# Optimization experiments

Hardware: AMD Instinct MI355X
Metric: run time of the kernel (lower is better)

## Reference

```python
import jax, jax.numpy as jnp
import numpy as np

B, S, DIM = 2, 2048, 2048
N_HEADS, N_KV_HEADS = 16, 4
HEAD_DIM = DIM // N_HEADS  # 128
N_REP = N_HEADS // N_KV_HEADS  # 4


def setup_inputs() -> dict:
    key = jax.random.key(0)
    ks = jax.random.split(key, 7)
    x = jax.random.normal(ks[0], (B, S, DIM), dtype=jnp.float32)
    cos = jax.random.uniform(ks[1], (S, HEAD_DIM // 2), dtype=jnp.float32)
    sin = jax.random.uniform(ks[2], (S, HEAD_DIM // 2), dtype=jnp.float32)
    sc = 1.0 / np.sqrt(DIM)
    wq = jax.random.normal(ks[3], (DIM, N_HEADS * HEAD_DIM), dtype=jnp.float32) * sc
    wk = jax.random.normal(ks[4], (DIM, N_KV_HEADS * HEAD_DIM), dtype=jnp.float32) * sc
    wv = jax.random.normal(ks[5], (DIM, N_KV_HEADS * HEAD_DIM), dtype=jnp.float32) * sc
    wo = jax.random.normal(ks[6], (N_HEADS * HEAD_DIM, DIM), dtype=jnp.float32) * sc
    return {"x": x, "cos": cos, "sin": sin, "wq": wq, "wk": wk, "wv": wv, "wo": wo}


def _rope(t, cos, sin):
    # t: [B, S, H, hd]; cos/sin: [S, hd/2] -> broadcast as [1, S, 1, hd/2]
    tr, ti = t[..., ::2], t[..., 1::2]
    c = cos[None, :, None, :]
    s = sin[None, :, None, :]
    out_r = tr * c - ti * s
    out_i = tr * s + ti * c
    # interleave back: stack on new last axis then flatten
    return jnp.stack([out_r, out_i], axis=-1).reshape(t.shape)


def reference(x, cos, sin, wq, wk, wv, wo):
    bsz, seqlen, _ = x.shape
    xq = (x @ wq).reshape(bsz, seqlen, N_HEADS, HEAD_DIM)
    xk = (x @ wk).reshape(bsz, seqlen, N_KV_HEADS, HEAD_DIM)
    xv = (x @ wv).reshape(bsz, seqlen, N_KV_HEADS, HEAD_DIM)
    xq = _rope(xq, cos, sin)
    xk = _rope(xk, cos, sin)
    # GQA: repeat kv heads -> [B, S, H, hd]
    xk = jnp.repeat(xk, N_REP, axis=2)
    xv = jnp.repeat(xv, N_REP, axis=2)
    scale = 1.0 / jnp.sqrt(jnp.asarray(HEAD_DIM, dtype=x.dtype))
    scores = jnp.einsum("bqhd,bkhd->bhqk", xq, xk) * scale
    causal = jnp.tril(jnp.ones((seqlen, seqlen), dtype=bool))
    scores = jnp.where(causal[None, None, :, :], scores, jnp.asarray(-jnp.inf, dtype=scores.dtype))
    attn = jax.nn.softmax(scores, axis=-1)
    out = jnp.einsum("bhqk,bkhd->bqhd", attn, xv)
    out = out.reshape(bsz, seqlen, N_HEADS * HEAD_DIM)
    return out @ wo
```

## Files before the change

kernel.cpp:

```cpp
#include <hip/hip_runtime.h>
#include <stdint.h>

#define SEQ 2048

typedef uint16_t u16;
typedef uint32_t u32;
typedef __attribute__((ext_vector_type(4))) float f32x4;
typedef __attribute__((ext_vector_type(8))) __bf16 bf16x8;
typedef __attribute__((ext_vector_type(4))) __bf16 bf16x4;

__device__ __forceinline__ u16 f2bf(float f) {
    u32 u = __float_as_uint(f);
    u += 0x7FFFu + ((u >> 16) & 1u);
    return (u16)(u >> 16);
}
__device__ __forceinline__ float bf2f(u16 h) {
    return __uint_as_float(((u32)h) << 16);
}
__device__ __forceinline__ u32 cvt_pk_bf16(float lo, float hi) {
    u32 r;
    asm("v_cvt_pk_bf16_f32 %0, %1, %2" : "=v"(r) : "v"(lo), "v"(hi));
    return r;
}
__device__ __forceinline__ void async16(const void* g, void* l) {
    auto gp = (__attribute__((address_space(1))) void*)const_cast<void*>(g);
    auto lp = (__attribute__((address_space(3))) void*)l;
    __builtin_amdgcn_global_load_lds(gp, lp, 16, 0, 0);
}

__global__ __launch_bounds__(256) void convert_bf16(const float* __restrict__ src,
                                                    u16* __restrict__ dst) {
    int i = blockIdx.x * 256 + threadIdx.x;
    float4 v = ((const float4*)src)[i];
    ((uint2*)dst)[i] = make_uint2(cvt_pk_bf16(v.x, v.y), cvt_pk_bf16(v.z, v.w));
}

__global__ __launch_bounds__(256) void tconv_all(const float* __restrict__ wq,
                                                 const float* __restrict__ wk,
                                                 const float* __restrict__ wv,
                                                 const float* __restrict__ wo,
                                                 u16* __restrict__ wqkvT,
                                                 u16* __restrict__ woT) {
    __shared__ float tile[64][65];
    const int bx = blockIdx.x, k0 = blockIdx.y * 64;
    const float* src; u16* dst; int N, n0;
    if (bx < 32)      { src = wq; dst = wqkvT;                        N = 2048; n0 = bx * 64; }
    else if (bx < 40) { src = wk; dst = wqkvT + (size_t)2048 * 2048;  N = 512;  n0 = (bx - 32) * 64; }
    else if (bx < 48) { src = wv; dst = wqkvT + (size_t)2560 * 2048;  N = 512;  n0 = (bx - 40) * 64; }
    else              { src = wo; dst = woT;                          N = 2048; n0 = (bx - 48) * 64; }
    const int tid = threadIdx.x;
#pragma unroll
    for (int p = 0; p < 4; p++) {
        int r = p * 16 + (tid >> 4);
        int c = (tid & 15) * 4;
        float4 v = *(const float4*)&src[(size_t)(k0 + r) * N + n0 + c];
        tile[r][c] = v.x; tile[r][c+1] = v.y; tile[r][c+2] = v.z; tile[r][c+3] = v.w;
    }
    __syncthreads();
#pragma unroll
    for (int p = 0; p < 4; p++) {
        int n = p * 16 + (tid >> 4);
        int kq = (tid & 15) * 4;
        u32 lo = cvt_pk_bf16(tile[kq+0][n], tile[kq+1][n]);
        u32 hi = cvt_pk_bf16(tile[kq+2][n], tile[kq+3][n]);
        *(uint2*)&dst[(size_t)(n0 + n) * 2048 + k0 + kq] = make_uint2(lo, hi);
    }
}

template <bool FUSE>
__global__ __launch_bounds__(256, 2) void gemm128(const u16* __restrict__ A,
                                                  const u16* __restrict__ Bt,
                                                  void* __restrict__ Cv,
                                                  int N, int K, int nbx,
                                                  const float* __restrict__ cosp,
                                                  const float* __restrict__ sinp,
                                                  u16* __restrict__ vt) {
    __shared__ u16 lds[4 * 8192];

    const int nwg = gridDim.x;
    const int q = nwg >> 3, r = nwg & 7;
    const int xcd = blockIdx.x & 7, lid = blockIdx.x >> 3;
    const int wg = (xcd < r ? xcd * (q + 1) : r * (q + 1) + (xcd - r) * q) + lid;
    const int by = wg / nbx, bx = wg - by * nbx;
    const int m0 = by * 128, n0 = bx * 128;

    const int tid = threadIdx.x;
    const int w = tid >> 6, l = tid & 63;
    const int lr = l & 15, quad = l >> 4;
    const int wm = (w >> 1) * 64, wn = (w & 1) * 64;
    const int cs = ((quad ^ (lr & 3) ^ ((lr >> 2) & 3)) & 3) * 8;

    const int sr = tid >> 2;
    const int sg = tid & 3;
    const int swz = (sr ^ (sr >> 2)) & 3;
    const u16* aS = A  + (size_t)(m0 + sr) * K + (sg ^ swz) * 8;
    const u16* bS = Bt + (size_t)(n0 + sr) * K + (sg ^ swz) * 8;
    u16* ldA = lds + tid * 8;
    u16* ldB = lds + 4096 + tid * 8;

    f32x4 acc[4][4] = {};
    const int nK = K >> 5;

    auto stage = [&](int kt) {
        u16* dA = ldA + (kt & 3) * 8192;
        u16* dB = ldB + (kt & 3) * 8192;
        const u16* sa = aS + (size_t)kt * 32;
        const u16* sb = bS + (size_t)kt * 32;
        async16(sa, dA);
        async16(sa + (size_t)64 * K, dA + 2048);
        async16(sb, dB);
        async16(sb + (size_t)64 * K, dB + 2048);
    };

    stage(0); stage(1); stage(2);
    asm volatile("s_waitcnt vmcnt(8)" ::: "memory");
    __builtin_amdgcn_s_barrier();

    for (int kt = 0; kt < nK; ++kt) {
        const u16* As = lds + (kt & 3) * 8192;
        const u16* Bs = As + 4096;
        bf16x8 af[4], bfr[4];
#pragma unroll
        for (int i = 0; i < 4; i++)
            af[i] = *(const bf16x8*)&As[(wm + i * 16 + lr) * 32 + cs];
#pragma unroll
        for (int i = 0; i < 4; i++)
            bfr[i] = *(const bf16x8*)&Bs[(wn + i * 16 + lr) * 32 + cs];
        if (kt + 3 < nK) stage(kt + 3);
        __builtin_amdgcn_s_barrier();
        asm volatile("s_waitcnt lgkmcnt(0)" ::: "memory");
        __builtin_amdgcn_s_setprio(1);
#pragma unroll
        for (int mf = 0; mf < 4; mf++)
#pragma unroll
            for (int nf = 0; nf < 4; nf++)
                acc[mf][nf] = __builtin_amdgcn_mfma_f32_16x16x32_bf16(af[mf], bfr[nf], acc[mf][nf], 0, 0, 0);
        __builtin_amdgcn_s_setprio(0);
        if (kt < nK - 3)       asm volatile("s_waitcnt vmcnt(8)" ::: "memory");
        else if (kt == nK - 3) asm volatile("s_waitcnt vmcnt(4)" ::: "memory");
        else if (kt == nK - 2) asm volatile("s_waitcnt vmcnt(0)" ::: "memory");
        if (kt < nK - 1) __builtin_amdgcn_s_barrier();
    }

    if constexpr (FUSE) {
        if (n0 >= 2560) {
            const int bb = m0 >> 11;
#pragma unroll
            for (int mf = 0; mf < 4; mf++) {
                const int token0 = (m0 + wm + mf * 16 + quad * 4) & (SEQ - 1);
#pragma unroll
                for (int nf = 0; nf < 4; nf++) {
                    int dg = n0 - 2560 + wn + nf * 16 + lr;
                    int kh = dg >> 7, d = dg & 127;
                    u32 lo = cvt_pk_bf16(acc[mf][nf][0], acc[mf][nf][1]);
                    u32 hi = cvt_pk_bf16(acc[mf][nf][2], acc[mf][nf][3]);
                    *(uint2*)&vt[((size_t)((bb * 4 + kh) * 128 + d)) * SEQ + token0] = make_uint2(lo, hi);
                }
            }
        } else if (n0 >= 2048) {
            const float sgn = (lr & 1) ? 1.0f : -1.0f;
#pragma unroll
            for (int mf = 0; mf < 4; mf++) {
#pragma unroll
                for (int nf = 0; nf < 4; nf++) {
                    int col = n0 + wn + nf * 16 + lr;
                    int ci = (col & 127) >> 1;
#pragma unroll
                    for (int rr = 0; rr < 4; rr++) {
                        size_t row = (size_t)(m0 + wm + mf * 16 + quad * 4 + rr);
                        int token = (int)row & (SEQ - 1);
                        float v = acc[mf][nf][rr];
                        float ppart = __shfl_xor(v, 1);
                        float c = cosp[token * 64 + ci];
                        float s = sinp[token * 64 + ci];
                        float ov = fmaf(sgn * ppart, s, v * c);
                        ((u16*)Cv)[row * (size_t)N + col] = f2bf(ov);
                    }
                }
            }
        } else {
#pragma unroll
            for (int mf = 0; mf < 4; mf++)
#pragma unroll
                for (int nf = 0; nf < 4; nf++)
#pragma unroll
                    for (int rr = 0; rr < 4; rr++) {
                        size_t row = (size_t)(m0 + wm + mf * 16 + quad * 4 + rr);
                        size_t col = (size_t)(n0 + wn + nf * 16 + lr);
                        ((u16*)Cv)[row * (size_t)N + col] = f2bf(acc[mf][nf][rr]);
                    }
        }
    } else {
#pragma unroll
        for (int mf = 0; mf < 4; mf++)
#pragma unroll
            for (int nf = 0; nf < 4; nf++)
#pragma unroll
                for (int rr = 0; rr < 4; rr++) {
                    size_t row = (size_t)(m0 + wm + mf * 16 + quad * 4 + rr);
                    size_t col = (size_t)(n0 + wn + nf * 16 + lr);
                    ((float*)Cv)[row * (size_t)N + col] = acc[mf][nf][rr];
                }
    }
}

__global__ __launch_bounds__(512, 2) void flash_attn(const u16* __restrict__ qkv,
                                                     const u16* __restrict__ vt,
                                                     const float* __restrict__ cosp,
                                                     const float* __restrict__ sinp,
                                                     u16* __restrict__ ob) {
    __shared__ u16 sh[65536];
    const int bidx = blockIdx.x;
    const int xcd   = bidx & 7;
    const int inner = bidx >> 3;
    const int b  = xcd >> 2, kh = xcd & 3;
    const int h  = kh * 4 + (inner & 3);
    const int a  = inner >> 2;
    const int tid = threadIdx.x;
    const int w = tid >> 6, lane = tid & 63;
    const int grp = w >> 2, wl = w & 3;
    const int lr = lane & 15, quad = lane >> 4;
    const float qscale = 0.088388347762f * 1.4426950408889634f;

    u16* base_g = sh + grp * 24576;
    u16* vb  = base_g + 16384;
    u16* lPw = sh + 49152 + w * 2048;

    const int tidg = tid & 255;
    const int krow = tidg >> 4;
    const int kchunk = (tidg & 15) ^ krow;
    const int vrow = tidg >> 3;
    const int vchunk = (tidg & 7) ^ (vrow & 7);
    const u16* kRow = qkv + (size_t)b * SEQ * 3072 + 2048 + kh * 128
                    + (size_t)krow * 3072 + kchunk * 8;
    const u16* vRow = vt + (size_t)(b * 4 + kh) * 128 * SEQ
                    + (size_t)vrow * SEQ + vchunk * 8;

    auto stageK = [&](int kt, int buf) {
        u16* d = base_g + buf * 8192 + tidg * 8;
#pragma unroll
        for (int i = 0; i < 4; i++)
            async16(kRow + (size_t)(kt * 64 + i * 16) * 3072, d + i * 2048);
    };
    auto stageV = [&](int kt) {
        u16* d = vb + tidg * 8;
#pragma unroll
        for (int i = 0; i < 4; i++)
            async16(vRow + (size_t)(i * 32) * SEQ + kt * 64, d + i * 2048);
    };

    float* mO = (float*)sh;
    float* mM = (float*)(sh + 49152);

    for (int p = 0; p < 2; p++) {
        const int qt = p ? (7 - a) : (8 + a);
        const int niters = p ? (8 - a) : (9 + a);
        const int kt0 = grp * niters;

        stageK(kt0, 0);

        bf16x8 qf[2][4];
#pragma unroll
        for (int qi = 0; qi < 2; qi++) {
            const int token = qt * 128 + wl * 32 + qi * 16 + lr;
            const u16* qb = qkv + (size_t)(b * SEQ + token) * 3072 + h * 128;
#pragma unroll
            for (int kk = 0; kk < 4; kk++) {
                uint4 raw = *(const uint4*)(qb + kk * 32 + quad * 8);
                u32 rw[4] = {raw.x, raw.y, raw.z, raw.w};
                union { u32 u[4]; bf16x8 v; } fr;
#pragma unroll
                for (int pp = 0; pp < 4; pp++) {
                    int ci = kk * 16 + quad * 4 + pp;
                    float cv = cosp[token * 64 + ci];
                    float sv = sinp[token * 64 + ci];
                    float tr = bf2f((u16)(rw[pp] & 0xFFFFu));
                    float ti = bf2f((u16)(rw[pp] >> 16));
                    fr.u[pp] = cvt_pk_bf16((tr * cv - ti * sv) * qscale,
                                           (tr * sv + ti * cv) * qscale);
                }
                qf[qi][kk] = fr.v;
            }
        }

        f32x4 o[2][8] = {};
        float m_st[2] = {-1e30f, -1e30f};
        float l_st[2] = {0.f, 0.f};
        const int qg = qt * 128 + wl * 32 + lr;

        for (int t = 0; t < niters; t++) {
            const int kt = kt0 + t;
            const int buf = t & 1;
            stageV(kt);
            if (t + 1 < niters) {
                stageK(kt + 1, buf ^ 1);
                asm volatile("s_waitcnt vmcnt(8)" ::: "memory");
            } else {
                asm volatile("s_waitcnt vmcnt(4)" ::: "memory");
            }
            asm volatile("s_barrier" ::: "memory");

            const u16* kcur = base_g + buf * 8192;
            f32x4 sc[2][4] = {};
            __builtin_amdgcn_s_setprio(1);
#pragma unroll
            for (int nf = 0; nf < 4; nf++) {
#pragma unroll
                for (int kk = 0; kk < 4; kk++) {
                    bf16x8 ak = *(const bf16x8*)&kcur[(nf * 16 + lr) * 128 + (((kk * 4 + quad) ^ lr) * 8)];
                    sc[0][nf] = __builtin_amdgcn_mfma_f32_16x16x32_bf16(ak, qf[0][kk], sc[0][nf], 0, 0, 0);
                    sc[1][nf] = __builtin_amdgcn_mfma_f32_16x16x32_bf16(ak, qf[1][kk], sc[1][nf], 0, 0, 0);
                }
            }
            __builtin_amdgcn_s_setprio(0);

            const int kb = kt * 64 + quad * 4;
            const int kmax = kt * 64 + 63;
#pragma unroll
            for (int qi = 0; qi < 2; qi++) {
                float ps[4][4];
                float tm[4];
                const int qrow_g = qg + qi * 16;
                if (kmax > qt * 128 + wl * 32 + qi * 16) {
#pragma unroll
                    for (int nf = 0; nf < 4; nf++) {
                        tm[nf] = -1e30f;
#pragma unroll
                        for (int r = 0; r < 4; r++) {
                            float v = sc[qi][nf][r];
                            if ((kb + nf * 16 + r) > qrow_g) v = -1e30f;
                            ps[nf][r] = v;
                            tm[nf] = fmaxf(tm[nf], v);
                        }
                    }
                } else {
#pragma unroll
                    for (int nf = 0; nf < 4; nf++) {
                        tm[nf] = -1e30f;
#pragma unroll
                        for (int r = 0; r < 4; r++) {
                            float v = sc[qi][nf][r];
                            ps[nf][r] = v;
                            tm[nf] = fmaxf(tm[nf], v);
                        }
                    }
                }
                float tmax = fmaxf(fmaxf(tm[0], tm[1]), fmaxf(tm[2], tm[3]));
                tmax = fmaxf(tmax, __shfl_xor(tmax, 16));
                tmax = fmaxf(tmax, __shfl_xor(tmax, 32));
                const float mprev = m_st[qi];
                if (!__all(tmax - mprev <= 8.0f)) {
                    float mnew = fmaxf(mprev, tmax);
                    float alpha = exp2f(mprev - mnew);
                    l_st[qi] *= alpha;
                    m_st[qi] = mnew;
#pragma unroll
                    for (int r = 0; r < 4; r++) {
                        float ar = __shfl(alpha, quad * 4 + r, 16);
#pragma unroll
                        for (int nd = 0; nd < 8; nd++) o[qi][nd][r] *= ar;
                    }
                }
                const float mcur = m_st[qi];
                float rs[4];
#pragma unroll
                for (int nf = 0; nf < 4; nf++) {
                    rs[nf] = 0.f;
#pragma unroll
                    for (int r = 0; r < 4; r++) {
                        float e = exp2f(ps[nf][r] - mcur);
                        ps[nf][r] = e;
                        rs[nf] += e;
                    }
                }
                float rsum = (rs[0] + rs[1]) + (rs[2] + rs[3]);
                rsum += __shfl_xor(rsum, 16);
                rsum += __shfl_xor(rsum, 32);
                l_st[qi] += rsum;
                const int qrow = qi * 16 + lr;
#pragma unroll
                for (int nf = 0; nf < 4; nf++) {
                    u32 lo = cvt_pk_bf16(ps[nf][0], ps[nf][1]);
                    u32 hi = cvt_pk_bf16(ps[nf][2], ps[nf][3]);
                    int c = (nf * 4 + quad) ^ lr;
                    *(uint2*)&lPw[qrow * 64 + c * 4] = make_uint2(lo, hi);
                }
            }

            if (t + 1 < niters) asm volatile("s_waitcnt vmcnt(4)" ::: "memory");
            else                asm volatile("s_waitcnt vmcnt(0)" ::: "memory");
            asm volatile("s_barrier" ::: "memory");

            __builtin_amdgcn_s_setprio(1);
#pragma unroll
            for (int kf = 0; kf < 2; kf++) {
                bf16x8 pa[2];
#pragma unroll
                for (int qi = 0; qi < 2; qi++) {
                    int c0 = (kf * 8 + quad * 2) ^ lr;
                    int c1 = (kf * 8 + quad * 2 + 1) ^ lr;
                    bf16x4 p0 = *(const bf16x4*)&lPw[(qi * 16 + lr) * 64 + c0 * 4];
                    bf16x4 p1 = *(const bf16x4*)&lPw[(qi * 16 + lr) * 64 + c1 * 4];
                    pa[qi] = __builtin_shufflevector(p0, p1, 0, 1, 2, 3, 4, 5, 6, 7);
                }
#pragma unroll
                for (int nd = 0; nd < 8; nd++) {
                    bf16x8 vv = *(const bf16x8*)&vb[(nd * 16 + lr) * 64 + (((kf * 4 + quad) ^ (lr & 7)) * 8)];
                    o[0][nd] = __builtin_amdgcn_mfma_f32_16x16x32_bf16(pa[0], vv, o[0][nd], 0, 0, 0);
                    o[1][nd] = __builtin_amdgcn_mfma_f32_16x16x32_bf16(pa[1], vv, o[1][nd], 0, 0, 0);
                }
            }
            __builtin_amdgcn_s_setprio(0);

            asm volatile("s_barrier" ::: "memory");
        }

        __syncthreads();
        if (grp == 1) {
#pragma unroll
            for (int qi = 0; qi < 2; qi++) {
#pragma unroll
                for (int r = 0; r < 4; r++) {
                    int row = wl * 32 + qi * 16 + quad * 4 + r;
#pragma unroll
                    for (int nd = 0; nd < 8; nd++)
                        mO[row * 128 + nd * 16 + lr] = o[qi][nd][r];
                }
                if (quad == 0) {
                    int rowl = wl * 32 + qi * 16 + lr;
                    mM[rowl * 2]     = m_st[qi];
                    mM[rowl * 2 + 1] = l_st[qi];
                }
            }
        }
        __syncthreads();
        if (grp == 0) {
#pragma unroll
            for (int qi = 0; qi < 2; qi++) {
                int rowl = wl * 32 + qi * 16 + lr;
                float m1 = mM[rowl * 2], l1 = mM[rowl * 2 + 1];
                float M  = fmaxf(m_st[qi], m1);
                float a0 = exp2f(m_st[qi] - M);
                float a1 = exp2f(m1 - M);
                float li = 1.0f / (l_st[qi] * a0 + l1 * a1);
                u16* obase = ob + (size_t)(b * SEQ + qt * 128 + wl * 32 + qi * 16) * 2048 + h * 128;
#pragma unroll
                for (int r = 0; r < 4; r++) {
                    float a0b = __shfl(a0, quad * 4 + r, 16);
                    float a1b = __shfl(a1, quad * 4 + r, 16);
                    float lib = __shfl(li, quad * 4 + r, 16);
                    int row = wl * 32 + qi * 16 + quad * 4 + r;
#pragma unroll
                    for (int nd = 0; nd < 8; nd++) {
                        float val = (o[qi][nd][r] * a0b + mO[row * 128 + nd * 16 + lr] * a1b) * lib;
                        obase[(quad * 4 + r) * 2048 + nd * 16 + lr] = f2bf(val);
                    }
                }
            }
        }
        __syncthreads();
    }
}

extern "C" void kernel_launch(void* const* d_in, const int* in_sizes, int n_in,
                              void* d_out, int out_size, void* d_ws, size_t ws_size,
                              hipStream_t stream) {
    (void)in_sizes; (void)n_in; (void)out_size; (void)ws_size;
    const float* x    = (const float*)d_in[0];
    const float* cosp = (const float*)d_in[1];
    const float* sinp = (const float*)d_in[2];
    const float* wq   = (const float*)d_in[3];
    const float* wk   = (const float*)d_in[4];
    const float* wv   = (const float*)d_in[5];
    const float* wo   = (const float*)d_in[6];
    float* out = (float*)d_out;

    char* ws = (char*)d_ws;
    u16* xb    = (u16*)(ws);
    u16* qkvb  = (u16*)(ws + (size_t)16 * 1024 * 1024);
    u16* wqkvT = (u16*)(ws + (size_t)40 * 1024 * 1024);
    u16* woT   = (u16*)(ws + (size_t)52 * 1024 * 1024);
    u16* vtb   = (u16*)(ws + (size_t)60 * 1024 * 1024);
    u16* ob    = xb;

    convert_bf16<<<8192, 256, 0, stream>>>(x, xb);
    tconv_all<<<dim3(80, 32), 256, 0, stream>>>(wq, wk, wv, wo, wqkvT, woT);
    gemm128<true><<<768, 256, 0, stream>>>(xb, wqkvT, (void*)qkvb, 3072, 2048, 24,
                                           cosp, sinp, vtb);
    flash_attn<<<256, 512, 0, stream>>>(qkvb, vtb, cosp, sinp, ob);
    gemm128<false><<<512, 256, 0, stream>>>(ob, woT, (void*)out, 2048, 2048, 16,
                                            nullptr, nullptr, nullptr);
}
```

Baseline: 308.4 us.

## Replace split-KV two-group attention blocks with one q-tile per 256-thread block

The attention kernel previously used 512-thread blocks in which two wave groups split the KV range of a query tile, handled two paired q-tiles per block for load balance, and merged partial results through shared memory. Now each 256-thread block handles one 128-row q-tile over the full causal KV range, with 512 blocks ordered so heavy and light tiles interleave. This removes the cross-group merge, the extra syncthreads and half the shared memory. In exchange, per-block work becomes unbalanced (from 2 to 32 iterations), so tail effects depend on how the scheduler packs blocks.

Result: no change. 311.7 us (+1.1%).

```diff
diff --git a/kernel.cpp b/kernel.cpp
--- a/kernel.cpp
+++ b/kernel.cpp
@@ -204,261 +204,220 @@
     }
 }
 
-__global__ __launch_bounds__(512, 2) void flash_attn(const u16* __restrict__ qkv,
+__global__ __launch_bounds__(256, 2) void flash_attn(const u16* __restrict__ qkv,
                                                      const u16* __restrict__ vt,
                                                      const float* __restrict__ cosp,
                                                      const float* __restrict__ sinp,
                                                      u16* __restrict__ ob) {
-    __shared__ u16 sh[65536];
+    __shared__ u16 sh[32768];
     const int bidx = blockIdx.x;
     const int xcd   = bidx & 7;
     const int inner = bidx >> 3;
     const int b  = xcd >> 2, kh = xcd & 3;
-    const int h  = kh * 4 + (inner & 3);
-    const int a  = inner >> 2;
+    const int c  = inner & 31;
+    const int qt = (inner >> 5) ? (15 - (c >> 2)) : (c >> 2);
+    const int h  = kh * 4 + (c & 3);
     const int tid = threadIdx.x;
     const int w = tid >> 6, lane = tid & 63;
-    const int grp = w >> 2, wl = w & 3;
     const int lr = lane & 15, quad = lane >> 4;
     const float qscale = 0.088388347762f * 1.4426950408889634f;
 
-    u16* base_g = sh + grp * 24576;
-    u16* vb  = base_g + 16384;
-    u16* lPw = sh + 49152 + w * 2048;
-
-    const int tidg = tid & 255;
-    const int krow = tidg >> 4;
-    const int kchunk = (tidg & 15) ^ krow;
-    const int vrow = tidg >> 3;
-    const int vchunk = (tidg & 7) ^ (vrow & 7);
+    u16* vb  = sh + 16384;
+    u16* lPw = sh + 24576 + w * 2048;
+
+    const int krow = tid >> 4;
+    const int kchunk = (tid & 15) ^ krow;
+    const int vrow = tid >> 3;
+    const int vchunk = (tid & 7) ^ (vrow & 7);
     const u16* kRow = qkv + (size_t)b * SEQ * 3072 + 2048 + kh * 128
                     + (size_t)krow * 3072 + kchunk * 8;
     const u16* vRow = vt + (size_t)(b * 4 + kh) * 128 * SEQ
                     + (size_t)vrow * SEQ + vchunk * 8;
 
     auto stageK = [&](int kt, int buf) {
-        u16* d = base_g + buf * 8192 + tidg * 8;
+        u16* d = sh + buf * 8192 + tid * 8;
 #pragma unroll
         for (int i = 0; i < 4; i++)
             async16(kRow + (size_t)(kt * 64 + i * 16) * 3072, d + i * 2048);
     };
     auto stageV = [&](int kt) {
-        u16* d = vb + tidg * 8;
+        u16* d = vb + tid * 8;
 #pragma unroll
         for (int i = 0; i < 4; i++)
             async16(vRow + (size_t)(i * 32) * SEQ + kt * 64, d + i * 2048);
     };
 
-    float* mO = (float*)sh;
-    float* mM = (float*)(sh + 49152);
-
-    for (int p = 0; p < 2; p++) {
-        const int qt = p ? (7 - a) : (8 + a);
-        const int niters = p ? (8 - a) : (9 + a);
-        const int kt0 = grp * niters;
-
-        stageK(kt0, 0);
-
-        bf16x8 qf[2][4];
+    const int niters = 2 * (qt + 1);
+
+    stageK(0, 0);
+
+    bf16x8 qf[2][4];
+#pragma unroll
+    for (int qi = 0; qi < 2; qi++) {
+        const int token = qt * 128 + w * 32 + qi * 16 + lr;
+        const u16* qb = qkv + (size_t)(b * SEQ + token) * 3072 + h * 128;
+#pragma unroll
+        for (int kk = 0; kk < 4; kk++) {
+            uint4 raw = *(const uint4*)(qb + kk * 32 + quad * 8);
+            u32 rw[4] = {raw.x, raw.y, raw.z, raw.w};
+            union { u32 u[4]; bf16x8 v; } fr;
+#pragma unroll
+            for (int pp = 0; pp < 4; pp++) {
+                int ci = kk * 16 + quad * 4 + pp;
+                float cv = cosp[token * 64 + ci];
+                float sv = sinp[token * 64 + ci];
+                float tr = bf2f((u16)(rw[pp] & 0xFFFFu));
+                float ti = bf2f((u16)(rw[pp] >> 16));
+                fr.u[pp] = cvt_pk_bf16((tr * cv - ti * sv) * qscale,
+                                       (tr * sv + ti * cv) * qscale);
+            }
+            qf[qi][kk] = fr.v;
+        }
+    }
+
+    f32x4 o[2][8] = {};
+    float m_st[2] = {-1e30f, -1e30f};
+    float l_st[2] = {0.f, 0.f};
+    const int qg = qt * 128 + w * 32 + lr;
+
+    for (int t = 0; t < niters; t++) {
+        const int kt = t;
+        const int buf = t & 1;
+        stageV(kt);
+        if (t + 1 < niters) {
+            stageK(kt + 1, buf ^ 1);
+            asm volatile("s_waitcnt vmcnt(8)" ::: "memory");
+        } else {
+            asm volatile("s_waitcnt vmcnt(4)" ::: "memory");
+        }
+        asm volatile("s_barrier" ::: "memory");
+
+        const u16* kcur = sh + buf * 8192;
+        f32x4 sc[2][4] = {};
+        __builtin_amdgcn_s_setprio(1);
+#pragma unroll
+        for (int nf = 0; nf < 4; nf++) {
+#pragma unroll
+            for (int kk = 0; kk < 4; kk++) {
+                bf16x8 ak = *(const bf16x8*)&kcur[(nf * 16 + lr) * 128 + (((kk * 4 + quad) ^ lr) * 8)];
+                sc[0][nf] = __builtin_amdgcn_mfma_f32_16x16x32_bf16(ak, qf[0][kk], sc[0][nf], 0, 0, 0);
+                sc[1][nf] = __builtin_amdgcn_mfma_f32_16x16x32_bf16(ak, qf[1][kk], sc[1][nf], 0, 0, 0);
+            }
+        }
+        __builtin_amdgcn_s_setprio(0);
+
+        const int kb = kt * 64 + quad * 4;
+        const int kmax = kt * 64 + 63;
 #pragma unroll
         for (int qi = 0; qi < 2; qi++) {
-            const int token = qt * 128 + wl * 32 + qi * 16 + lr;
-            const u16* qb = qkv + (size_t)(b * SEQ + token) * 3072 + h * 128;
-#pragma unroll
-            for (int kk = 0; kk < 4; kk++) {
-                uint4 raw = *(const uint4*)(qb + kk * 32 + quad * 8);
-                u32 rw[4] = {raw.x, raw.y, raw.z, raw.w};
-                union { u32 u[4]; bf16x8 v; } fr;
-#pragma unroll
-                for (int pp = 0; pp < 4; pp++) {
-                    int ci = kk * 16 + quad * 4 + pp;
-                    float cv = cosp[token * 64 + ci];
-                    float sv = sinp[token * 64 + ci];
-                    float tr = bf2f((u16)(rw[pp] & 0xFFFFu));
-                    float ti = bf2f((u16)(rw[pp] >> 16));
-                    fr.u[pp] = cvt_pk_bf16((tr * cv - ti * sv) * qscale,
-                                           (tr * sv + ti * cv) * qscale);
-                }
-                qf[qi][kk] = fr.v;
-            }
-        }
-
-        f32x4 o[2][8] = {};
-        float m_st[2] = {-1e30f, -1e30f};
-        float l_st[2] = {0.f, 0.f};
-        const int qg = qt * 128 + wl * 32 + lr;
-
-        for (int t = 0; t < niters; t++) {
-            const int kt = kt0 + t;
-            const int buf = t & 1;
-            stageV(kt);
-            if (t + 1 < niters) {
-                stageK(kt + 1, buf ^ 1);
-                asm volatile("s_waitcnt vmcnt(8)" ::: "memory");
+            float ps[4][4];
+            float tm[4];
+            const int qrow_g = qg + qi * 16;
+            if (kmax > qt * 128 + w * 32 + qi * 16) {
+#pragma unroll
+                for (int nf = 0; nf < 4; nf++) {
+                    tm[nf] = -1e30f;
+#pragma unroll
+                    for (int r = 0; r < 4; r++) {
+                        float v = sc[qi][nf][r];
+                        if ((kb + nf * 16 + r) > qrow_g) v = -1e30f;
+                        ps[nf][r] = v;
+                        tm[nf] = fmaxf(tm[nf], v);
+                    }
+                }
             } else {
-                asm volatile("s_waitcnt vmcnt(4)" ::: "memory");
-            }
-            asm volatile("s_barrier" ::: "memory");
-
-            const u16* kcur = base_g + buf * 8192;
-            f32x4 sc[2][4] = {};
-            __builtin_amdgcn_s_setprio(1);
+#pragma unroll
+                for (int nf = 0; nf < 4; nf++) {
+                    tm[nf] = -1e30f;
+#pragma unroll
+                    for (int r = 0; r < 4; r++) {
+                        float v = sc[qi][nf][r];
+                        ps[nf][r] = v;
+                        tm[nf] = fmaxf(tm[nf], v);
+                    }
+                }
+            }
+            float tmax = fmaxf(fmaxf(tm[0], tm[1]), fmaxf(tm[2], tm[3]));
+            tmax = fmaxf(tmax, __shfl_xor(tmax, 16));
+            tmax = fmaxf(tmax, __shfl_xor(tmax, 32));
+            const float mprev = m_st[qi];
+            if (!__all(tmax - mprev <= 8.0f)) {
+                float mnew = fmaxf(mprev, tmax);
+                float alpha = exp2f(mprev - mnew);
+                l_st[qi] *= alpha;
+                m_st[qi] = mnew;
+#pragma unroll
+                for (int r = 0; r < 4; r++) {
+                    float ar = __shfl(alpha, quad * 4 + r, 16);
+#pragma unroll
+                    for (int nd = 0; nd < 8; nd++) o[qi][nd][r] *= ar;
+                }
+            }
+            const float mcur = m_st[qi];
+            float rs[4];
 #pragma unroll
             for (int nf = 0; nf < 4; nf++) {
-#pragma unroll
-                for (int kk = 0; kk < 4; kk++) {
-                    bf16x8 ak = *(const bf16x8*)&kcur[(nf * 16 + lr) * 128 + (((kk * 4 + quad) ^ lr) * 8)];
-                    sc[0][nf] = __builtin_amdgcn_mfma_f32_16x16x32_bf16(ak, qf[0][kk], sc[0][nf], 0, 0, 0);
-                    sc[1][nf] = __builtin_amdgcn_mfma_f32_16x16x32_bf16(ak, qf[1][kk], sc[1][nf], 0, 0, 0);
-                }
-            }
-            __builtin_amdgcn_s_setprio(0);
-
-            const int kb = kt * 64 + quad * 4;
-            const int kmax = kt * 64 + 63;
+                rs[nf] = 0.f;
+#pragma unroll
+                for (int r = 0; r < 4; r++) {
+                    float e = exp2f(ps[nf][r] - mcur);
+                    ps[nf][r] = e;
+                    rs[nf] += e;
+                }
+            }
+            float rsum = (rs[0] + rs[1]) + (rs[2] + rs[3]);
+            rsum += __shfl_xor(rsum, 16);
+            rsum += __shfl_xor(rsum, 32);
+            l_st[qi] += rsum;
+            const int qrow = qi * 16 + lr;
+#pragma unroll
+            for (int nf = 0; nf < 4; nf++) {
+                u32 lo = cvt_pk_bf16(ps[nf][0], ps[nf][1]);
+                u32 hi = cvt_pk_bf16(ps[nf][2], ps[nf][3]);
+                int cc = (nf * 4 + quad) ^ lr;
+                *(uint2*)&lPw[qrow * 64 + cc * 4] = make_uint2(lo, hi);
+            }
+        }
+
+        if (t + 1 < niters) asm volatile("s_waitcnt vmcnt(4)" ::: "memory");
+        else                asm volatile("s_waitcnt vmcnt(0)" ::: "memory");
+        asm volatile("s_barrier" ::: "memory");
+
+        __builtin_amdgcn_s_setprio(1);
+#pragma unroll
+        for (int kf = 0; kf < 2; kf++) {
+            bf16x8 pa[2];
 #pragma unroll
             for (int qi = 0; qi < 2; qi++) {
-                float ps[4][4];
-                float tm[4];
-                const int qrow_g = qg + qi * 16;
-                if (kmax > qt * 128 + wl * 32 + qi * 16) {
-#pragma unroll
-                    for (int nf = 0; nf < 4; nf++) {
-                        tm[nf] = -1e30f;
-#pragma unroll
-                        for (int r = 0; r < 4; r++) {
-                            float v = sc[qi][nf][r];
-                            if ((kb + nf * 16 + r) > qrow_g) v = -1e30f;
-                            ps[nf][r] = v;
-                            tm[nf] = fmaxf(tm[nf], v);
-                        }
-                    }
-                } else {
-#pragma unroll
-                    for (int nf = 0; nf < 4; nf++) {
-                        tm[nf] = -1e30f;
-#pragma unroll
-                        for (int r = 0; r < 4; r++) {
-                            float v = sc[qi][nf][r];
-                            ps[nf][r] = v;
-                            tm[nf] = fmaxf(tm[nf], v);
-                        }
-                    }
-                }
-                float tmax = fmaxf(fmaxf(tm[0], tm[1]), fmaxf(tm[2], tm[3]));
-                tmax = fmaxf(tmax, __shfl_xor(tmax, 16));
-                tmax = fmaxf(tmax, __shfl_xor(tmax, 32));
-                const float mprev = m_st[qi];
-                if (!__all(tmax - mprev <= 8.0f)) {
-                    float mnew = fmaxf(mprev, tmax);
-                    float alpha = exp2f(mprev - mnew);
-                    l_st[qi] *= alpha;
-                    m_st[qi] = mnew;
-#pragma unroll
-                    for (int r = 0; r < 4; r++) {
-                        float ar = __shfl(alpha, quad * 4 + r, 16);
-#pragma unroll
-                        for (int nd = 0; nd < 8; nd++) o[qi][nd][r] *= ar;
-                    }
-                }
-                const float mcur = m_st[qi];
-                float rs[4];
-#pragma unroll
-                for (int nf = 0; nf < 4; nf++) {
-                    rs[nf] = 0.f;
-#pragma unroll
-                    for (int r = 0; r < 4; r++) {
-                        float e = exp2f(ps[nf][r] - mcur);
-                        ps[nf][r] = e;
-                        rs[nf] += e;
-                    }
-                }
-                float rsum = (rs[0] + rs[1]) + (rs[2] + rs[3]);
-                rsum += __shfl_xor(rsum, 16);
-                rsum += __shfl_xor(rsum, 32);
-                l_st[qi] += rsum;
-                const int qrow = qi * 16 + lr;
-#pragma unroll
-                for (int nf = 0; nf < 4; nf++) {
-                    u32 lo = cvt_pk_bf16(ps[nf][0], ps[nf][1]);
-                    u32 hi = cvt_pk_bf16(ps[nf][2], ps[nf][3]);
-                    int c = (nf * 4 + quad) ^ lr;
-                    *(uint2*)&lPw[qrow * 64 + c * 4] = make_uint2(lo, hi);
-                }
-            }
-
-            if (t + 1 < niters) asm volatile("s_waitcnt vmcnt(4)" ::: "memory");
-            else                asm volatile("s_waitcnt vmcnt(0)" ::: "memory");
-            asm volatile("s_barrier" ::: "memory");
-
-            __builtin_amdgcn_s_setprio(1);
-#pragma unroll
-            for (int kf = 0; kf < 2; kf++) {
-                bf16x8 pa[2];
-#pragma unroll
-                for (int qi = 0; qi < 2; qi++) {
-                    int c0 = (kf * 8 + quad * 2) ^ lr;
-                    int c1 = (kf * 8 + quad * 2 + 1) ^ lr;
-                    bf16x4 p0 = *(const bf16x4*)&lPw[(qi * 16 + lr) * 64 + c0 * 4];
-                    bf16x4 p1 = *(const bf16x4*)&lPw[(qi * 16 + lr) * 64 + c1 * 4];
-                    pa[qi] = __builtin_shufflevector(p0, p1, 0, 1, 2, 3, 4, 5, 6, 7);
-                }
-#pragma unroll
-                for (int nd = 0; nd < 8; nd++) {
-                    bf16x8 vv = *(const bf16x8*)&vb[(nd * 16 + lr) * 64 + (((kf * 4 + quad) ^ (lr & 7)) * 8)];
-                    o[0][nd] = __builtin_amdgcn_mfma_f32_16x16x32_bf16(pa[0], vv, o[0][nd], 0, 0, 0);
-                    o[1][nd] = __builtin_amdgcn_mfma_f32_16x16x32_bf16(pa[1], vv, o[1][nd], 0, 0, 0);
-                }
-            }
-            __builtin_amdgcn_s_setprio(0);
-
-            asm volatile("s_barrier" ::: "memory");
-        }
-
-        __syncthreads();
-        if (grp == 1) {
-#pragma unroll
-            for (int qi = 0; qi < 2; qi++) {
-#pragma unroll
-                for (int r = 0; r < 4; r++) {
-                    int row = wl * 32 + qi * 16 + quad * 4 + r;
-#pragma unroll
-                    for (int nd = 0; nd < 8; nd++)
-                        mO[row * 128 + nd * 16 + lr] = o[qi][nd][r];
-                }
-                if (quad == 0) {
-                    int rowl = wl * 32 + qi * 16 + lr;
-                    mM[rowl * 2]     = m_st[qi];
-                    mM[rowl * 2 + 1] = l_st[qi];
-                }
-            }
-        }
-        __syncthreads();
-        if (grp == 0) {
-#pragma unroll
-            for (int qi = 0; qi < 2; qi++) {
-                int rowl = wl * 32 + qi * 16 + lr;
-                float m1 = mM[rowl * 2], l1 = mM[rowl * 2 + 1];
-                float M  = fmaxf(m_st[qi], m1);
-                float a0 = exp2f(m_st[qi] - M);
-                float a1 = exp2f(m1 - M);
-                float li = 1.0f / (l_st[qi] * a0 + l1 * a1);
-                u16* obase = ob + (size_t)(b * SEQ + qt * 128 + wl * 32 + qi * 16) * 2048 + h * 128;
-#pragma unroll
-                for (int r = 0; r < 4; r++) {
-                    float a0b = __shfl(a0, quad * 4 + r, 16);
-                    float a1b = __shfl(a1, quad * 4 + r, 16);
-                    float lib = __shfl(li, quad * 4 + r, 16);
-                    int row = wl * 32 + qi * 16 + quad * 4 + r;
-#pragma unroll
-                    for (int nd = 0; nd < 8; nd++) {
-                        float val = (o[qi][nd][r] * a0b + mO[row * 128 + nd * 16 + lr] * a1b) * lib;
-                        obase[(quad * 4 + r) * 2048 + nd * 16 + lr] = f2bf(val);
-                    }
-                }
-            }
-        }
-        __syncthreads();
+                int c0 = (kf * 8 + quad * 2) ^ lr;
+                int c1 = (kf * 8 + quad * 2 + 1) ^ lr;
+                bf16x4 p0 = *(const bf16x4*)&lPw[(qi * 16 + lr) * 64 + c0 * 4];
+                bf16x4 p1 = *(const bf16x4*)&lPw[(qi * 16 + lr) * 64 + c1 * 4];
+                pa[qi] = __builtin_shufflevector(p0, p1, 0, 1, 2, 3, 4, 5, 6, 7);
+            }
+#pragma unroll
+            for (int nd = 0; nd < 8; nd++) {
+                bf16x8 vv = *(const bf16x8*)&vb[(nd * 16 + lr) * 64 + (((kf * 4 + quad) ^ (lr & 7)) * 8)];
+                o[0][nd] = __builtin_amdgcn_mfma_f32_16x16x32_bf16(pa[0], vv, o[0][nd], 0, 0, 0);
+                o[1][nd] = __builtin_amdgcn_mfma_f32_16x16x32_bf16(pa[1], vv, o[1][nd], 0, 0, 0);
+            }
+        }
+        __builtin_amdgcn_s_setprio(0);
+
+        asm volatile("s_barrier" ::: "memory");
+    }
+
+#pragma unroll
+    for (int qi = 0; qi < 2; qi++) {
+        float li = 1.0f / l_st[qi];
+        u16* obase = ob + (size_t)(b * SEQ + qt * 128 + w * 32 + qi * 16) * 2048 + h * 128;
+#pragma unroll
+        for (int r = 0; r < 4; r++) {
+            float lib = __shfl(li, quad * 4 + r, 16);
+#pragma unroll
+            for (int nd = 0; nd < 8; nd++)
+                obase[(quad * 4 + r) * 2048 + nd * 16 + lr] = f2bf(o[qi][nd][r] * lib);
+        }
     }
 }
 
@@ -487,7 +446,7 @@
     tconv_all<<<dim3(80, 32), 256, 0, stream>>>(wq, wk, wv, wo, wqkvT, woT);
     gemm128<true><<<768, 256, 0, stream>>>(xb, wqkvT, (void*)qkvb, 3072, 2048, 24,
                                            cosp, sinp, vtb);
-    flash_attn<<<256, 512, 0, stream>>>(qkvb, vtb, cosp, sinp, ob);
+    flash_attn<<<512, 256, 0, stream>>>(qkvb, vtb, cosp, sinp, ob);
     gemm128<false><<<512, 256, 0, stream>>>(ob, woT, (void*)out, 2048, 2048, 16,
                                             nullptr, nullptr, nullptr);
 }
```

## Switch GEMMs to 256x256 tiles with 8 waves and double-buffered K=64 stages

Applied to the files above, without the earlier changes.

Replaces the 128x128, 4-wave GEMM with a 256x256 tile computed by 8 waves, each owning a 128x64 sub-tile. K is split into 64-wide double-buffered steps with interleaved A/B half-stage loads between MFMA batches. The larger tile raises arithmetic intensity and cuts global and LDS traffic per FLOP. The cost is far fewer workgroups (192 and 128 on a chip with 256 CUs), which leaves some compute units idle, plus more registers and 128KB of LDS per block, limiting occupancy.

Result: slower. 317.2 us (+2.9%).

```diff
diff --git a/kernel.cpp b/kernel.cpp
--- a/kernel.cpp
+++ b/kernel.cpp
@@ -68,108 +68,147 @@
 }
 
 template <bool FUSE>
-__global__ __launch_bounds__(256, 2) void gemm128(const u16* __restrict__ A,
-                                                  const u16* __restrict__ Bt,
-                                                  void* __restrict__ Cv,
-                                                  int N, int K, int nbx,
-                                                  const float* __restrict__ cosp,
-                                                  const float* __restrict__ sinp,
-                                                  u16* __restrict__ vt) {
-    __shared__ u16 lds[4 * 8192];
+__global__ __launch_bounds__(512, 2) void gemm8(const u16* __restrict__ A,
+                                                const u16* __restrict__ Bt,
+                                                void* __restrict__ Cv,
+                                                int N, int K, int nbx,
+                                                const float* __restrict__ cosp,
+                                                const float* __restrict__ sinp,
+                                                u16* __restrict__ vt) {
+    __shared__ u16 lds[65536];
 
     const int nwg = gridDim.x;
     const int q = nwg >> 3, r = nwg & 7;
     const int xcd = blockIdx.x & 7, lid = blockIdx.x >> 3;
     const int wg = (xcd < r ? xcd * (q + 1) : r * (q + 1) + (xcd - r) * q) + lid;
     const int by = wg / nbx, bx = wg - by * nbx;
-    const int m0 = by * 128, n0 = bx * 128;
+    const int m0 = by * 256, n0 = bx * 256;
 
     const int tid = threadIdx.x;
     const int w = tid >> 6, l = tid & 63;
     const int lr = l & 15, quad = l >> 4;
-    const int wm = (w >> 1) * 64, wn = (w & 1) * 64;
+    const int wm = (w >> 2) * 128;
+    const int wn = (w & 3) * 64;
     const int cs = ((quad ^ (lr & 3) ^ ((lr >> 2) & 3)) & 3) * 8;
 
-    const int sr = tid >> 2;
-    const int sg = tid & 3;
-    const int swz = (sr ^ (sr >> 2)) & 3;
-    const u16* aS = A  + (size_t)(m0 + sr) * K + (sg ^ swz) * 8;
-    const u16* bS = Bt + (size_t)(n0 + sr) * K + (sg ^ swz) * 8;
-    u16* ldA = lds + tid * 8;
-    u16* ldB = lds + 4096 + tid * 8;
-
-    f32x4 acc[4][4] = {};
-    const int nK = K >> 5;
-
-    auto stage = [&](int kt) {
-        u16* dA = ldA + (kt & 3) * 8192;
-        u16* dB = ldB + (kt & 3) * 8192;
-        const u16* sa = aS + (size_t)kt * 32;
-        const u16* sb = bS + (size_t)kt * 32;
-        async16(sa, dA);
-        async16(sa + (size_t)64 * K, dA + 2048);
-        async16(sb, dB);
-        async16(sb + (size_t)64 * K, dB + 2048);
+    const int r0 = tid >> 2, g0 = tid & 3;
+    const int kg = g0 ^ ((r0 ^ (r0 >> 2)) & 3);
+    const u16* aSrc = A  + (size_t)(m0 + r0) * K + kg * 8;
+    const u16* bSrc = Bt + (size_t)(n0 + r0) * K + kg * 8;
+
+    auto stageA = [&](int kt, int ks) {
+        u16* d = lds + (kt & 1) * 32768 + ks * 8192 + tid * 8;
+        const u16* s = aSrc + (size_t)kt * 64 + ks * 32;
+        async16(s, d);
+        async16(s + (size_t)128 * K, d + 4096);
     };
-
-    stage(0); stage(1); stage(2);
-    asm volatile("s_waitcnt vmcnt(8)" ::: "memory");
-    __builtin_amdgcn_s_barrier();
-
-    for (int kt = 0; kt < nK; ++kt) {
-        const u16* As = lds + (kt & 3) * 8192;
-        const u16* Bs = As + 4096;
+    auto stageB = [&](int kt, int ks) {
+        u16* d = lds + (kt & 1) * 32768 + 16384 + ks * 8192 + tid * 8;
+        const u16* s = bSrc + (size_t)kt * 64 + ks * 32;
+        async16(s, d);
+        async16(s + (size_t)128 * K, d + 4096);
+    };
+
+    f32x4 acc[8][4] = {};
+    const int nK = K >> 6;
+
+    stageA(0, 0); stageB(0, 0); stageA(0, 1); stageB(0, 1);
+    stageA(1, 0); stageB(1, 0);
+
+    for (int u = 0; u < nK; ++u) {
+        const u16* Ab = lds + (u & 1) * 32768;
+        const u16* Bb = Ab + 16384;
         bf16x8 af[4], bfr[4];
-#pragma unroll
-        for (int i = 0; i < 4; i++)
-            af[i] = *(const bf16x8*)&As[(wm + i * 16 + lr) * 32 + cs];
-#pragma unroll
-        for (int i = 0; i < 4; i++)
-            bfr[i] = *(const bf16x8*)&Bs[(wn + i * 16 + lr) * 32 + cs];
-        if (kt + 3 < nK) stage(kt + 3);
+
+        if (u < nK - 2) asm volatile("s_waitcnt vmcnt(6)" ::: "memory");
+        else            asm volatile("s_waitcnt vmcnt(0)" ::: "memory");
         __builtin_amdgcn_s_barrier();
+#pragma unroll
+        for (int i = 0; i < 4; i++) af[i]  = *(const bf16x8*)&Ab[(wm + i * 16 + lr) * 32 + cs];
+#pragma unroll
+        for (int j = 0; j < 4; j++) bfr[j] = *(const bf16x8*)&Bb[(wn + j * 16 + lr) * 32 + cs];
+        if (u + 1 < nK) stageA(u + 1, 1);
         asm volatile("s_waitcnt lgkmcnt(0)" ::: "memory");
         __builtin_amdgcn_s_setprio(1);
 #pragma unroll
-        for (int mf = 0; mf < 4; mf++)
-#pragma unroll
-            for (int nf = 0; nf < 4; nf++)
-                acc[mf][nf] = __builtin_amdgcn_mfma_f32_16x16x32_bf16(af[mf], bfr[nf], acc[mf][nf], 0, 0, 0);
+        for (int i = 0; i < 4; i++)
+#pragma unroll
+            for (int j = 0; j < 4; j++)
+                acc[i][j] = __builtin_amdgcn_mfma_f32_16x16x32_bf16(af[i], bfr[j], acc[i][j], 0, 0, 0);
         __builtin_amdgcn_s_setprio(0);
-        if (kt < nK - 3)       asm volatile("s_waitcnt vmcnt(8)" ::: "memory");
-        else if (kt == nK - 3) asm volatile("s_waitcnt vmcnt(4)" ::: "memory");
-        else if (kt == nK - 2) asm volatile("s_waitcnt vmcnt(0)" ::: "memory");
-        if (kt < nK - 1) __builtin_amdgcn_s_barrier();
+
+        __builtin_amdgcn_s_barrier();
+#pragma unroll
+        for (int i = 0; i < 4; i++) af[i] = *(const bf16x8*)&Ab[(wm + 64 + i * 16 + lr) * 32 + cs];
+        if (u + 1 < nK) stageB(u + 1, 1);
+        asm volatile("s_waitcnt lgkmcnt(0)" ::: "memory");
+        __builtin_amdgcn_s_setprio(1);
+#pragma unroll
+        for (int i = 0; i < 4; i++)
+#pragma unroll
+            for (int j = 0; j < 4; j++)
+                acc[4 + i][j] = __builtin_amdgcn_mfma_f32_16x16x32_bf16(af[i], bfr[j], acc[4 + i][j], 0, 0, 0);
+        __builtin_amdgcn_s_setprio(0);
+
+        if (u < nK - 2) asm volatile("s_waitcnt vmcnt(6)" ::: "memory");
+        else            asm volatile("s_waitcnt vmcnt(0)" ::: "memory");
+        __builtin_amdgcn_s_barrier();
+#pragma unroll
+        for (int i = 0; i < 4; i++) af[i]  = *(const bf16x8*)&Ab[8192 + (wm + i * 16 + lr) * 32 + cs];
+#pragma unroll
+        for (int j = 0; j < 4; j++) bfr[j] = *(const bf16x8*)&Bb[8192 + (wn + j * 16 + lr) * 32 + cs];
+        if (u + 2 < nK) stageA(u + 2, 0);
+        asm volatile("s_waitcnt lgkmcnt(0)" ::: "memory");
+        __builtin_amdgcn_s_setprio(1);
+#pragma unroll
+        for (int i = 0; i < 4; i++)
+#pragma unroll
+            for (int j = 0; j < 4; j++)
+                acc[i][j] = __builtin_amdgcn_mfma_f32_16x16x32_bf16(af[i], bfr[j], acc[i][j], 0, 0, 0);
+        __builtin_amdgcn_s_setprio(0);
+
+        __builtin_amdgcn_s_barrier();
+#pragma unroll
+        for (int i = 0; i < 4; i++) af[i] = *(const bf16x8*)&Ab[8192 + (wm + 64 + i * 16 + lr) * 32 + cs];
+        if (u + 2 < nK) stageB(u + 2, 0);
+        asm volatile("s_waitcnt lgkmcnt(0)" ::: "memory");
+        __builtin_amdgcn_s_setprio(1);
+#pragma unroll
+        for (int i = 0; i < 4; i++)
+#pragma unroll
+            for (int j = 0; j < 4; j++)
+                acc[4 + i][j] = __builtin_amdgcn_mfma_f32_16x16x32_bf16(af[i], bfr[j], acc[4 + i][j], 0, 0, 0);
+        __builtin_amdgcn_s_setprio(0);
     }
 
     if constexpr (FUSE) {
         if (n0 >= 2560) {
             const int bb = m0 >> 11;
 #pragma unroll
-            for (int mf = 0; mf < 4; mf++) {
-                const int token0 = (m0 + wm + mf * 16 + quad * 4) & (SEQ - 1);
+            for (int a = 0; a < 8; a++) {
+                const int token0 = (m0 + wm + (a >> 2) * 64 + (a & 3) * 16 + quad * 4) & (SEQ - 1);
 #pragma unroll
                 for (int nf = 0; nf < 4; nf++) {
                     int dg = n0 - 2560 + wn + nf * 16 + lr;
                     int kh = dg >> 7, d = dg & 127;
-                    u32 lo = cvt_pk_bf16(acc[mf][nf][0], acc[mf][nf][1]);
-                    u32 hi = cvt_pk_bf16(acc[mf][nf][2], acc[mf][nf][3]);
+                    u32 lo = cvt_pk_bf16(acc[a][nf][0], acc[a][nf][1]);
+                    u32 hi = cvt_pk_bf16(acc[a][nf][2], acc[a][nf][3]);
                     *(uint2*)&vt[((size_t)((bb * 4 + kh) * 128 + d)) * SEQ + token0] = make_uint2(lo, hi);
                 }
             }
         } else if (n0 >= 2048) {
             const float sgn = (lr & 1) ? 1.0f : -1.0f;
 #pragma unroll
-            for (int mf = 0; mf < 4; mf++) {
+            for (int a = 0; a < 8; a++) {
 #pragma unroll
                 for (int nf = 0; nf < 4; nf++) {
                     int col = n0 + wn + nf * 16 + lr;
                     int ci = (col & 127) >> 1;
 #pragma unroll
                     for (int rr = 0; rr < 4; rr++) {
-                        size_t row = (size_t)(m0 + wm + mf * 16 + quad * 4 + rr);
+                        size_t row = (size_t)(m0 + wm + (a >> 2) * 64 + (a & 3) * 16 + quad * 4 + rr);
                         int token = (int)row & (SEQ - 1);
-                        float v = acc[mf][nf][rr];
+                        float v = acc[a][nf][rr];
                         float ppart = __shfl_xor(v, 1);
                         float c = cosp[token * 64 + ci];
                         float s = sinp[token * 64 + ci];
@@ -180,26 +219,26 @@
             }
         } else {
 #pragma unroll
-            for (int mf = 0; mf < 4; mf++)
+            for (int a = 0; a < 8; a++)
 #pragma unroll
                 for (int nf = 0; nf < 4; nf++)
 #pragma unroll
                     for (int rr = 0; rr < 4; rr++) {
-                        size_t row = (size_t)(m0 + wm + mf * 16 + quad * 4 + rr);
+                        size_t row = (size_t)(m0 + wm + (a >> 2) * 64 + (a & 3) * 16 + quad * 4 + rr);
                         size_t col = (size_t)(n0 + wn + nf * 16 + lr);
-                        ((u16*)Cv)[row * (size_t)N + col] = f2bf(acc[mf][nf][rr]);
+                        ((u16*)Cv)[row * (size_t)N + col] = f2bf(acc[a][nf][rr]);
                     }
         }
     } else {
 #pragma unroll
-        for (int mf = 0; mf < 4; mf++)
+        for (int a = 0; a < 8; a++)
 #pragma unroll
             for (int nf = 0; nf < 4; nf++)
 #pragma unroll
                 for (int rr = 0; rr < 4; rr++) {
-                    size_t row = (size_t)(m0 + wm + mf * 16 + quad * 4 + rr);
+                    size_t row = (size_t)(m0 + wm + (a >> 2) * 64 + (a & 3) * 16 + quad * 4 + rr);
                     size_t col = (size_t)(n0 + wn + nf * 16 + lr);
-                    ((float*)Cv)[row * (size_t)N + col] = acc[mf][nf][rr];
+                    ((float*)Cv)[row * (size_t)N + col] = acc[a][nf][rr];
                 }
     }
 }
@@ -485,9 +524,9 @@
 
     convert_bf16<<<8192, 256, 0, stream>>>(x, xb);
     tconv_all<<<dim3(80, 32), 256, 0, stream>>>(wq, wk, wv, wo, wqkvT, woT);
-    gemm128<true><<<768, 256, 0, stream>>>(xb, wqkvT, (void*)qkvb, 3072, 2048, 24,
-                                           cosp, sinp, vtb);
+    gemm8<true><<<192, 512, 0, stream>>>(xb, wqkvT, (void*)qkvb, 3072, 2048, 12,
+                                         cosp, sinp, vtb);
     flash_attn<<<256, 512, 0, stream>>>(qkvb, vtb, cosp, sinp, ob);
-    gemm128<false><<<512, 256, 0, stream>>>(ob, woT, (void*)out, 2048, 2048, 16,
-                                            nullptr, nullptr, nullptr);
-}
+    gemm8<false><<<128, 512, 0, stream>>>(ob, woT, (void*)out, 2048, 2048, 8,
+                                          nullptr, nullptr, nullptr);
+}
```
